# Kernel optimization log

Hardware: AMD Instinct MI355X
Metric: run time of the kernel (lower is better)

Reference implementation:

```python
import math
import jax, jax.numpy as jnp
import numpy as np

B, N, F, K = 4, 4096, 128, 32
EPS = 1e-8  # tsl.epsilon
TEMP0, TEMP_DECAY = 1.0, 0.99995


def setup_inputs() -> dict:
    key = jax.random.key(0)
    k1, k2, k3, k4 = jax.random.split(key, 4)
    emb = jax.random.normal(k1, (B, N, F), dtype=jnp.float32)
    adj = jax.random.uniform(k2, (B, N, N), dtype=jnp.float32)
    logits_param = jax.random.normal(k3, (N, K), dtype=jnp.float32)
    u = jax.random.uniform(k4, (B, N, K), dtype=jnp.float32, minval=1e-9, maxval=1.0)
    gumbel_noise = -jnp.log(-jnp.log(u))
    return {"emb": emb, "adj": adj, "logits_param": logits_param, "gumbel_noise": gumbel_noise}


def reference(emb, adj, logits_param, gumbel_noise):
    # temp decays on each get_temp() call in training mode (called twice per forward)
    t1 = max(TEMP0 * TEMP_DECAY, 0.05)
    t2 = max(t1 * TEMP_DECAY, 0.05)

    # ---- gumbel-softmax hard sample with straight-through estimator ----
    y_soft = jax.nn.softmax(logits_param[None] / t1 + gumbel_noise, axis=-1)  # [B,N,K]
    y_hard = jax.nn.one_hot(jnp.argmax(y_soft, axis=-1), K, dtype=y_soft.dtype)
    s_sample = jax.lax.stop_gradient(y_hard - y_soft) + y_soft + EPS  # [B,N,K]

    # ---- soft assignment for regularizers (unbatched [N,K]) ----
    s_soft = jax.nn.softmax(logits_param / t2, axis=-1)  # [N,K]

    # mincut_num = trace(s^T A s) per batch, without forming [K,K]
    As = jnp.einsum('bnm,mk->bnk', adj, s_soft)            # [B,N,K]
    mincut_num = jnp.einsum('nk,bnk->b', s_soft, As)       # [B]
    # mincut_den = trace(s^T D s): D is diag(deg) -> O(N*K) instead of diag_embed
    d_flat = adj.sum(axis=-1)                              # [B,N]
    mincut_den = jnp.einsum('bn,nk,nk->b', d_flat, s_soft, s_soft)
    mincut_loss = -jnp.mean(mincut_num / mincut_den)

    ss = s_soft.T @ s_soft                                 # [K,K]
    ortho_loss = jnp.linalg.norm(ss / jnp.linalg.norm(ss) - jnp.eye(K, dtype=ss.dtype) / math.sqrt(K))

    # ---- pooling ----
    out_emb = jnp.einsum('bnk,bnf->bkf', s_sample, emb)    # [B,K,F]
    As2 = jnp.einsum('bnm,bml->bnl', adj, s_sample)        # [B,N,K]
    out_adj = jnp.einsum('bnk,bnl->bkl', s_sample, As2)    # [B,K,K]

    out_adj = out_adj * (1.0 - jnp.eye(K, dtype=out_adj.dtype))  # zero diagonal
    d = jnp.sqrt(out_adj.sum(axis=-1, keepdims=True)) + EPS
    out_adj = out_adj / d / jnp.swapaxes(d, -1, -2)

    return out_emb, out_adj, s_sample, mincut_loss, ortho_loss
```

## Files before the change

kernel.cpp:

```cpp
#include <hip/hip_runtime.h>
#include <hip/hip_bf16.h>
#include <math.h>

#define B_ 4
#define N_ 4096
#define F_ 128
#define K_ 32
#define EPS_ 1e-8f

typedef __attribute__((ext_vector_type(8))) __bf16 bf16x8;
typedef __attribute__((ext_vector_type(4))) float f32x4;

#define WS_SSOFT   0
#define WS_SQ      131072
#define WS_SS      135168
#define WS_WF      136192
#define WS_OADJP   660480
#define WS_NUMDEN  1709056
#define WS_PEMB    1711104
#define WS_OADJ    2235392
#define WS_H       2239488

__global__ void k_ssoft(const float* __restrict__ logits, float* __restrict__ s_soft,
                        float* __restrict__ sq, float* __restrict__ ss, float t2) {
  __shared__ float sl[64][33];
  int t = threadIdx.x;
  int rowbase = blockIdx.x * 64;
  if (t < 64) {
    int n = rowbase + t;
    float z[32];
    float mx = -1e30f;
    for (int k = 0; k < 32; ++k) { z[k] = logits[n*32+k] / t2; mx = fmaxf(mx, z[k]); }
    float s = 0.f;
    for (int k = 0; k < 32; ++k) { z[k] = expf(z[k]-mx); s += z[k]; }
    float sqa = 0.f;
    for (int k = 0; k < 32; ++k) {
      float v = z[k] / s;
      s_soft[n*32+k] = v;
      sl[t][k] = v;
      sqa += v*v;
    }
    sq[n] = sqa;
  }
  __syncthreads();
  for (int pp = 0; pp < 4; ++pp) {
    int p = pp*256 + t;
    int k = p >> 5, l = p & 31;
    float a = 0.f;
    for (int r = 0; r < 64; ++r) a += sl[r][k]*sl[r][l];
    atomicAdd(&ss[p], a);
  }
}

__global__ void k_gumbel(const float* __restrict__ logits, const float* __restrict__ gum,
                         float* __restrict__ s_sample, int* __restrict__ h, float t1) {
  int i = blockIdx.x*256 + threadIdx.x;
  int n = i & (N_-1);
  float z[32];
  float mx = -1e30f;
  for (int k = 0; k < 32; ++k) { z[k] = logits[n*32+k]/t1 + gum[(size_t)i*32+k]; mx = fmaxf(mx, z[k]); }
  float s = 0.f;
  for (int k = 0; k < 32; ++k) { z[k] = expf(z[k]-mx); s += z[k]; }
  int am = 0; float best = -1.f;
  for (int k = 0; k < 32; ++k) { z[k] = z[k]/s; if (z[k] > best) { best = z[k]; am = k; } }
  for (int k = 0; k < 32; ++k) {
    float yh = (k==am) ? 1.f : 0.f;
    s_sample[(size_t)i*32+k] = (yh - z[k]) + z[k] + EPS_;
  }
  h[i] = am;
}

__global__ void k_wfrag(const float* __restrict__ s_soft, const int* __restrict__ h,
                        bf16x8* __restrict__ wf) {
  int i = blockIdx.x*256 + threadIdx.x;
  int lane = i & 63;
  int c = (i >> 6) & 3;
  int tt = (i >> 8) & 127;
  int b = i >> 15;
  int col = c*16 + (lane & 15);
  int m0 = tt*32 + (lane >> 4)*8;
  bf16x8 v;
  if (col < 32) {
    for (int j = 0; j < 8; ++j) v[j] = (__bf16)s_soft[(m0+j)*32 + col];
  } else {
    int cc = col - 32;
    for (int j = 0; j < 8; ++j) v[j] = (__bf16)((h[b*N_ + m0 + j] == cc) ? 1.f : 0.f);
  }
  wf[i] = v;
}

#define NT(p) __builtin_nontemporal_load((const f32x4*)(p))

__launch_bounds__(256, 4)
__global__ void k_gemm(const float* __restrict__ adj, const bf16x8* __restrict__ wf,
                       const float* __restrict__ s_soft, const float* __restrict__ sq,
                       const int* __restrict__ h, float* __restrict__ numden_p,
                       float* __restrict__ oadjp) {
  __shared__ float oal[1024];
  __shared__ float rn[4], rd[4];
  int t = threadIdx.x;
  int w = t >> 6, l = t & 63;
  int lr = l & 15, lhi = l >> 4;
  int bid = blockIdx.x;
  int sp = bid & 7, r = (bid >> 3) & 31, b = bid >> 8;

  for (int i = t; i < 1024; i += 256) oal[i] = 0.f;
  __syncthreads();

  int row0 = r*128;
  int m0 = sp*512;
  int rowA = row0 + w*32 + lr;

  const float* pA0 = adj + (size_t)b*N_*N_ + (size_t)rowA*N_ + m0 + lhi*8;
  const float* pA1 = pA0 + (size_t)16*N_;
  const bf16x8* pw = wf + ((size_t)b*128 + (m0 >> 5))*256 + l;

  f32x4 acc00 = {0,0,0,0}, acc01 = {0,0,0,0}, acc02 = {0,0,0,0}, acc03 = {0,0,0,0};
  f32x4 acc10 = {0,0,0,0}, acc11 = {0,0,0,0}, acc12 = {0,0,0,0}, acc13 = {0,0,0,0};

  f32x4 a0lo = NT(pA0), a0hi = NT(pA0 + 4);
  f32x4 a1lo = NT(pA1), a1hi = NT(pA1 + 4);
  bf16x8 wc0 = pw[0], wc1 = pw[64], wc2 = pw[128], wc3 = pw[192];

  #pragma unroll 1
  for (int c = 0; c < 16; ++c) {
    f32x4 n0lo, n0hi, n1lo, n1hi;
    bf16x8 wn0, wn1, wn2, wn3;
    if (c < 15) {
      pA0 += 32; pA1 += 32; pw += 256;
      n0lo = NT(pA0); n0hi = NT(pA0 + 4);
      n1lo = NT(pA1); n1hi = NT(pA1 + 4);
      wn0 = pw[0]; wn1 = pw[64]; wn2 = pw[128]; wn3 = pw[192];
    }
    bf16x8 fa0, fa1;
    #pragma unroll
    for (int j = 0; j < 4; ++j) {
      fa0[j]   = (__bf16)a0lo[j];
      fa0[j+4] = (__bf16)a0hi[j];
      fa1[j]   = (__bf16)a1lo[j];
      fa1[j+4] = (__bf16)a1hi[j];
    }
    acc00 = __builtin_amdgcn_mfma_f32_16x16x32_bf16(fa0, wc0, acc00, 0, 0, 0);
    acc01 = __builtin_amdgcn_mfma_f32_16x16x32_bf16(fa0, wc1, acc01, 0, 0, 0);
    acc02 = __builtin_amdgcn_mfma_f32_16x16x32_bf16(fa0, wc2, acc02, 0, 0, 0);
    acc03 = __builtin_amdgcn_mfma_f32_16x16x32_bf16(fa0, wc3, acc03, 0, 0, 0);
    acc10 = __builtin_amdgcn_mfma_f32_16x16x32_bf16(fa1, wc0, acc10, 0, 0, 0);
    acc11 = __builtin_amdgcn_mfma_f32_16x16x32_bf16(fa1, wc1, acc11, 0, 0, 0);
    acc12 = __builtin_amdgcn_mfma_f32_16x16x32_bf16(fa1, wc2, acc12, 0, 0, 0);
    acc13 = __builtin_amdgcn_mfma_f32_16x16x32_bf16(fa1, wc3, acc13, 0, 0, 0);
    if (c < 15) {
      a0lo = n0lo; a0hi = n0hi; a1lo = n1lo; a1hi = n1hi;
      wc0 = wn0; wc1 = wn1; wc2 = wn2; wc3 = wn3;
    }
  }

  float numacc = 0.f, denacc = 0.f;
  {
    f32x4 a0s[2] = {acc00, acc10}, a1s[2] = {acc01, acc11};
    f32x4 a2s[2] = {acc02, acc12}, a3s[2] = {acc03, acc13};
    int wrow0 = row0 + w*32;
    #pragma unroll
    for (int rt = 0; rt < 2; ++rt) {
      int rbase = wrow0 + rt*16 + lhi*4;
      #pragma unroll
      for (int i = 0; i < 4; ++i) {
        int row = rbase + i;
        float sqv = sq[row];
        int hv = h[b*N_ + row];
        numacc += a0s[rt][i] * s_soft[row*32 + lr];
        numacc += a1s[rt][i] * s_soft[row*32 + 16 + lr];
        float v2 = a2s[rt][i], v3 = a3s[rt][i];
        denacc += (v2 + v3) * sqv;
        atomicAdd(&oal[hv*32 + lr], v2);
        atomicAdd(&oal[hv*32 + 16 + lr], v3);
      }
    }
  }
  for (int off = 32; off; off >>= 1) {
    numacc += __shfl_down(numacc, off);
    denacc += __shfl_down(denacc, off);
  }
  if (l == 0) { rn[w] = numacc; rd[w] = denacc; }
  __syncthreads();
  if (t == 0) {
    numden_p[bid] = rn[0]+rn[1]+rn[2]+rn[3];
    numden_p[1024 + bid] = rd[0]+rd[1]+rd[2]+rd[3];
  }
  for (int i = t; i < 1024; i += 256) oadjp[(size_t)bid*1024 + i] = oal[i];
}

__global__ void k_outemb(const float* __restrict__ emb, const int* __restrict__ h,
                         float* __restrict__ pemb) {
  __shared__ float accl[32*128];
  int t = threadIdx.x;
  for (int i = t; i < 4096; i += 256) accl[i] = 0.f;
  __syncthreads();
  int b = blockIdx.x >> 5;
  int n0 = (blockIdx.x & 31) * 128;
  int f = t & 127, rr = t >> 7;
  for (int it = 0; it < 64; ++it) {
    int n = n0 + it*2 + rr;
    float v = emb[((size_t)b*N_ + n)*F_ + f];
    int hv = h[b*N_ + n];
    atomicAdd(&accl[hv*128 + f], v);
  }
  __syncthreads();
  for (int i = t; i < 4096; i += 256) pemb[(size_t)blockIdx.x*4096 + i] = accl[i];
}

__global__ void k_reduce(const float* __restrict__ oadjp, const float* __restrict__ pemb,
                         float* __restrict__ oadj, float* __restrict__ out_emb) {
  int blk = blockIdx.x;
  if (blk < 16) {
    int i = blk*256 + threadIdx.x;
    int b = i >> 10, ii = i & 1023;
    float s = 0.f;
    const float* p = oadjp + (size_t)(b*256)*1024 + ii;
    for (int j = 0; j < 256; ++j) s += p[(size_t)j*1024];
    oadj[i] = s;
  } else {
    int i = (blk-16)*256 + threadIdx.x;
    int b = i >> 12, ii = i & 4095;
    float s = 0.f;
    const float* p = pemb + (size_t)(b*32)*4096 + ii;
    for (int j = 0; j < 32; ++j) s += p[(size_t)j*4096];
    out_emb[i] = s;
  }
}

__global__ void k_final(const float* __restrict__ numden_p, const float* __restrict__ oadj,
                        const float* __restrict__ ss, float* __restrict__ dout) {
  __shared__ float dsh[128];
  __shared__ float red[256];
  __shared__ float nd[8];
  int t = threadIdx.x;
  if (t < 8) {
    int b = t & 3;
    const float* p = numden_p + (t >> 2)*1024 + b*256;
    float s = 0.f;
    for (int j = 0; j < 256; ++j) s += p[j];
    nd[t] = s;
  }
  if (t >= 64 && t < 192) {
    int i = t - 64;
    int b = i >> 5, k = i & 31;
    float s = 0.f;
    for (int l = 0; l < 32; ++l) if (l != k) s += oadj[b*1024 + k*32 + l];
    dsh[i] = sqrtf(s) + EPS_;
  }
  __syncthreads();
  for (int i = t; i < 4096; i += 256) {
    int b = i >> 10, k = (i >> 5) & 31, l = i & 31;
    float v = (k == l) ? 0.f : oadj[i] / (dsh[b*32+k] * dsh[b*32+l]);
    dout[16384 + i] = v;
  }
  float a = 0.f;
  for (int i = t; i < 1024; i += 256) { float v = ss[i]; a += v*v; }
  red[t] = a; __syncthreads();
  for (int s2 = 128; s2; s2 >>= 1) { if (t < s2) red[t] += red[t+s2]; __syncthreads(); }
  float fro = sqrtf(red[0]);
  __syncthreads();
  float c = 0.f;
  float inv = 1.f / fro;
  float dk = (float)(1.0 / sqrt(32.0));
  for (int i = t; i < 1024; i += 256) {
    int k = i >> 5, l = i & 31;
    float v = ss[i]*inv - ((k == l) ? dk : 0.f);
    c += v*v;
  }
  red[t] = c; __syncthreads();
  for (int s2 = 128; s2; s2 >>= 1) { if (t < s2) red[t] += red[t+s2]; __syncthreads(); }
  if (t == 0) {
    dout[544769] = sqrtf(red[0]);
    float s = 0.f;
    for (int b = 0; b < 4; ++b) s += nd[b] / nd[4+b];
    dout[544768] = -s*0.25f;
  }
}

extern "C" void kernel_launch(void* const* d_in, const int* in_sizes, int n_in,
                              void* d_out, int out_size, void* d_ws, size_t ws_size,
                              hipStream_t stream) {
  const float* emb    = (const float*)d_in[0];
  const float* adj    = (const float*)d_in[1];
  const float* logits = (const float*)d_in[2];
  const float* gum    = (const float*)d_in[3];
  float* out = (float*)d_out;
  float* ws  = (float*)d_ws;

  float t1 = 0.99995f;
  float t2 = (float)(0.99995 * 0.99995);

  float* s_soft = ws + WS_SSOFT;
  float* sq     = ws + WS_SQ;
  float* ss     = ws + WS_SS;
  bf16x8* wf    = (bf16x8*)(ws + WS_WF);
  float* oadjp  = ws + WS_OADJP;
  float* ndp    = ws + WS_NUMDEN;
  float* pemb   = ws + WS_PEMB;
  float* oadj   = ws + WS_OADJ;
  int* hbuf     = (int*)(ws + WS_H);

  (void)hipMemsetAsync(ss, 0, 1024 * sizeof(float), stream);

  k_ssoft <<<64, 256, 0, stream>>>(logits, s_soft, sq, ss, t2);
  k_gumbel<<<64, 256, 0, stream>>>(logits, gum, out + 20480, hbuf, t1);
  k_wfrag <<<512, 256, 0, stream>>>(s_soft, hbuf, wf);
  k_gemm  <<<1024, 256, 0, stream>>>(adj, wf, s_soft, sq, hbuf, ndp, oadjp);
  k_outemb<<<128, 256, 0, stream>>>(emb, hbuf, pemb);
  k_reduce<<<80, 256, 0, stream>>>(oadjp, pemb, oadj, out);
  k_final <<<1, 256, 0, stream>>>(ndp, oadj, ss, out);
}
```

Baseline: 440.2 us.

## Fuse soft-assign, gumbel sampling and fragment packing into one pre-kernel

Merges the s_soft, gumbel hard-sample and bf16 fragment-packing kernels into a single k_pre kernel that builds the MFMA weight fragments straight from shared memory. This removes two launches and a global round trip. The s_soft fragments are now stored once instead of per batch, so the GEMM reads a smaller shared weight array plus a per-batch one-hot array. The out_emb scatter kernel also switches to twice as many blocks covering 64 rows each, which doubles the partial sums the reduce kernel has to add up.

```diff
diff --git a/kernel.cpp b/kernel.cpp
--- a/kernel.cpp
+++ b/kernel.cpp
@@ -14,20 +14,27 @@
 #define WS_SSOFT   0
 #define WS_SQ      131072
 #define WS_SS      135168
-#define WS_WF      136192
-#define WS_OADJP   660480
-#define WS_NUMDEN  1709056
-#define WS_PEMB    1711104
-#define WS_OADJ    2235392
-#define WS_H       2239488
-
-__global__ void k_ssoft(const float* __restrict__ logits, float* __restrict__ s_soft,
-                        float* __restrict__ sq, float* __restrict__ ss, float t2) {
+#define WS_WFS     136192
+#define WS_WFH     201728
+#define WS_OADJP   463872
+#define WS_NUMDEN  1512448
+#define WS_PEMB    1514496
+#define WS_OADJ    2563072
+#define WS_H       2567168
+
+__global__ void k_pre(const float* __restrict__ logits, const float* __restrict__ gum,
+                      float* __restrict__ s_soft, float* __restrict__ sq,
+                      float* __restrict__ ss, float* __restrict__ s_sample,
+                      int* __restrict__ h, bf16x8* __restrict__ wfs,
+                      bf16x8* __restrict__ wfh, float t1, float t2) {
   __shared__ float sl[64][33];
+  __shared__ int hl[4][64];
   int t = threadIdx.x;
-  int rowbase = blockIdx.x * 64;
+  int r = blockIdx.x;
+  int n0 = r * 64;
+
   if (t < 64) {
-    int n = rowbase + t;
+    int n = n0 + t;
     float z[32];
     float mx = -1e30f;
     for (int k = 0; k < 32; ++k) { z[k] = logits[n*32+k] / t2; mx = fmaxf(mx, z[k]); }
@@ -42,57 +49,67 @@
     }
     sq[n] = sqa;
   }
-  __syncthreads();
+
+  {
+    int b = t >> 6, nn = t & 63;
+    int n = n0 + nn;
+    size_t i = (size_t)b * N_ + n;
+    float z[32];
+    float mx = -1e30f;
+    for (int k = 0; k < 32; ++k) { z[k] = logits[n*32+k]/t1 + gum[i*32+k]; mx = fmaxf(mx, z[k]); }
+    float s = 0.f;
+    for (int k = 0; k < 32; ++k) { z[k] = expf(z[k]-mx); s += z[k]; }
+    int am = 0; float best = -1.f;
+    for (int k = 0; k < 32; ++k) { z[k] = z[k]/s; if (z[k] > best) { best = z[k]; am = k; } }
+    for (int k = 0; k < 32; ++k) {
+      float yh = (k==am) ? 1.f : 0.f;
+      s_sample[i*32+k] = (yh - z[k]) + z[k] + EPS_;
+    }
+    h[i] = am;
+    hl[b][nn] = am;
+  }
+  __syncthreads();
+
   for (int pp = 0; pp < 4; ++pp) {
     int p = pp*256 + t;
     int k = p >> 5, l = p & 31;
     float a = 0.f;
-    for (int r = 0; r < 64; ++r) a += sl[r][k]*sl[r][l];
+    for (int rr = 0; rr < 64; ++rr) a += sl[rr][k]*sl[rr][l];
     atomicAdd(&ss[p], a);
   }
-}
-
-__global__ void k_gumbel(const float* __restrict__ logits, const float* __restrict__ gum,
-                         float* __restrict__ s_sample, int* __restrict__ h, float t1) {
-  int i = blockIdx.x*256 + threadIdx.x;
-  int n = i & (N_-1);
-  float z[32];
-  float mx = -1e30f;
-  for (int k = 0; k < 32; ++k) { z[k] = logits[n*32+k]/t1 + gum[(size_t)i*32+k]; mx = fmaxf(mx, z[k]); }
-  float s = 0.f;
-  for (int k = 0; k < 32; ++k) { z[k] = expf(z[k]-mx); s += z[k]; }
-  int am = 0; float best = -1.f;
-  for (int k = 0; k < 32; ++k) { z[k] = z[k]/s; if (z[k] > best) { best = z[k]; am = k; } }
-  for (int k = 0; k < 32; ++k) {
-    float yh = (k==am) ? 1.f : 0.f;
-    s_sample[(size_t)i*32+k] = (yh - z[k]) + z[k] + EPS_;
-  }
-  h[i] = am;
-}
-
-__global__ void k_wfrag(const float* __restrict__ s_soft, const int* __restrict__ h,
-                        bf16x8* __restrict__ wf) {
-  int i = blockIdx.x*256 + threadIdx.x;
-  int lane = i & 63;
-  int c = (i >> 6) & 3;
-  int tt = (i >> 8) & 127;
-  int b = i >> 15;
-  int col = c*16 + (lane & 15);
-  int m0 = tt*32 + (lane >> 4)*8;
-  bf16x8 v;
-  if (col < 32) {
-    for (int j = 0; j < 8; ++j) v[j] = (__bf16)s_soft[(m0+j)*32 + col];
-  } else {
-    int cc = col - 32;
-    for (int j = 0; j < 8; ++j) v[j] = (__bf16)((h[b*N_ + m0 + j] == cc) ? 1.f : 0.f);
-  }
-  wf[i] = v;
+
+  {
+    int lane = t & 63;
+    int c = (t >> 6) & 1;
+    int tts = t >> 7;
+    int col = c*16 + (lane & 15);
+    int lrow = tts*32 + (lane >> 4)*8;
+    bf16x8 v;
+    #pragma unroll
+    for (int j = 0; j < 8; ++j) v[j] = (__bf16)sl[lrow+j][col];
+    wfs[((size_t)(2*r + tts)*2 + c)*64 + lane] = v;
+  }
+
+  for (int it = 0; it < 4; ++it) {
+    int p = it*256 + t;
+    int lane = p & 63;
+    int c = (p >> 6) & 1;
+    int tts = (p >> 7) & 1;
+    int b = p >> 8;
+    int cc = c*16 + (lane & 15);
+    int lrow = tts*32 + (lane >> 4)*8;
+    bf16x8 v;
+    #pragma unroll
+    for (int j = 0; j < 8; ++j) v[j] = (__bf16)((hl[b][lrow+j] == cc) ? 1.f : 0.f);
+    wfh[(((size_t)b*(N_/32) + 2*r + tts)*2 + c)*64 + lane] = v;
+  }
 }
 
 #define NT(p) __builtin_nontemporal_load((const f32x4*)(p))
 
 __launch_bounds__(256, 4)
-__global__ void k_gemm(const float* __restrict__ adj, const bf16x8* __restrict__ wf,
+__global__ void k_gemm(const float* __restrict__ adj, const bf16x8* __restrict__ wfs,
+                       const bf16x8* __restrict__ wfh,
                        const float* __restrict__ s_soft, const float* __restrict__ sq,
                        const int* __restrict__ h, float* __restrict__ numden_p,
                        float* __restrict__ oadjp) {
@@ -113,24 +130,25 @@
 
   const float* pA0 = adj + (size_t)b*N_*N_ + (size_t)rowA*N_ + m0 + lhi*8;
   const float* pA1 = pA0 + (size_t)16*N_;
-  const bf16x8* pw = wf + ((size_t)b*128 + (m0 >> 5))*256 + l;
+  const bf16x8* pws = wfs + (size_t)(m0 >> 5)*128 + l;
+  const bf16x8* pwh = wfh + ((size_t)b*(N_/32) + (m0 >> 5))*128 + l;
 
   f32x4 acc00 = {0,0,0,0}, acc01 = {0,0,0,0}, acc02 = {0,0,0,0}, acc03 = {0,0,0,0};
   f32x4 acc10 = {0,0,0,0}, acc11 = {0,0,0,0}, acc12 = {0,0,0,0}, acc13 = {0,0,0,0};
 
   f32x4 a0lo = NT(pA0), a0hi = NT(pA0 + 4);
   f32x4 a1lo = NT(pA1), a1hi = NT(pA1 + 4);
-  bf16x8 wc0 = pw[0], wc1 = pw[64], wc2 = pw[128], wc3 = pw[192];
+  bf16x8 wc0 = pws[0], wc1 = pws[64], wc2 = pwh[0], wc3 = pwh[64];
 
   #pragma unroll 1
   for (int c = 0; c < 16; ++c) {
     f32x4 n0lo, n0hi, n1lo, n1hi;
     bf16x8 wn0, wn1, wn2, wn3;
     if (c < 15) {
-      pA0 += 32; pA1 += 32; pw += 256;
+      pA0 += 32; pA1 += 32; pws += 128; pwh += 128;
       n0lo = NT(pA0); n0hi = NT(pA0 + 4);
       n1lo = NT(pA1); n1hi = NT(pA1 + 4);
-      wn0 = pw[0]; wn1 = pw[64]; wn2 = pw[128]; wn3 = pw[192];
+      wn0 = pws[0]; wn1 = pws[64]; wn2 = pwh[0]; wn3 = pwh[64];
     }
     bf16x8 fa0, fa1;
     #pragma unroll
@@ -195,10 +213,10 @@
   int t = threadIdx.x;
   for (int i = t; i < 4096; i += 256) accl[i] = 0.f;
   __syncthreads();
-  int b = blockIdx.x >> 5;
-  int n0 = (blockIdx.x & 31) * 128;
+  int b = blockIdx.x >> 6;
+  int n0 = (blockIdx.x & 63) * 64;
   int f = t & 127, rr = t >> 7;
-  for (int it = 0; it < 64; ++it) {
+  for (int it = 0; it < 32; ++it) {
     int n = n0 + it*2 + rr;
     float v = emb[((size_t)b*N_ + n)*F_ + f];
     int hv = h[b*N_ + n];
@@ -222,8 +240,8 @@
     int i = (blk-16)*256 + threadIdx.x;
     int b = i >> 12, ii = i & 4095;
     float s = 0.f;
-    const float* p = pemb + (size_t)(b*32)*4096 + ii;
-    for (int j = 0; j < 32; ++j) s += p[(size_t)j*4096];
+    const float* p = pemb + (size_t)(b*64)*4096 + ii;
+    for (int j = 0; j < 64; ++j) s += p[(size_t)j*4096];
     out_emb[i] = s;
   }
 }
@@ -294,7 +312,8 @@
   float* s_soft = ws + WS_SSOFT;
   float* sq     = ws + WS_SQ;
   float* ss     = ws + WS_SS;
-  bf16x8* wf    = (bf16x8*)(ws + WS_WF);
+  bf16x8* wfs   = (bf16x8*)(ws + WS_WFS);
+  bf16x8* wfh   = (bf16x8*)(ws + WS_WFH);
   float* oadjp  = ws + WS_OADJP;
   float* ndp    = ws + WS_NUMDEN;
   float* pemb   = ws + WS_PEMB;
@@ -303,11 +322,9 @@
 
   (void)hipMemsetAsync(ss, 0, 1024 * sizeof(float), stream);
 
-  k_ssoft <<<64, 256, 0, stream>>>(logits, s_soft, sq, ss, t2);
-  k_gumbel<<<64, 256, 0, stream>>>(logits, gum, out + 20480, hbuf, t1);
-  k_wfrag <<<512, 256, 0, stream>>>(s_soft, hbuf, wf);
-  k_gemm  <<<1024, 256, 0, stream>>>(adj, wf, s_soft, sq, hbuf, ndp, oadjp);
-  k_outemb<<<128, 256, 0, stream>>>(emb, hbuf, pemb);
+  k_pre   <<<64, 256, 0, stream>>>(logits, gum, s_soft, sq, ss, out + 20480, hbuf, wfs, wfh, t1, t2);
+  k_gemm  <<<1024, 256, 0, stream>>>(adj, wfs, wfh, s_soft, sq, hbuf, ndp, oadjp);
+  k_outemb<<<256, 256, 0, stream>>>(emb, hbuf, pemb);
   k_reduce<<<80, 256, 0, stream>>>(oadjp, pemb, oadj, out);
   k_final <<<1, 256, 0, stream>>>(ndp, oadj, ss, out);
 }
```

Result: faster. 424.9 us (-3.5%).
